# Optimization experiments

Hardware: AMD Instinct MI355X
Metric: run time of the kernel (lower is better)

Reference implementation:

```python
import jax, jax.numpy as jnp
import numpy as np

N = 12000
E = 384000
F_IN, F_HID, F_OUT = 4, 50, 1433
NEG_SLOPE = 0.2  # PyG GATConv default leaky_relu slope


def gat_conv(x, W, a_src, a_dst, b, src, dst):
    """PyG GATConv (heads=1, concat=True) with self-loops already appended.
    x: [N, Fin], W: [Fin, Fout], a_src/a_dst/b: [Fout], src/dst: [E']."""
    h = x @ W                                   # [N, Fout]
    al = h @ a_src                              # [N] per-source logit part
    ar = h @ a_dst                              # [N] per-target logit part
    e = jax.nn.leaky_relu(al[src] + ar[dst], NEG_SLOPE)   # [E'] edge logits
    # segment softmax over edges grouped by destination node
    m = jax.ops.segment_max(e, dst, num_segments=N)       # [N]
    ex = jnp.exp(e - m[dst])
    s = jax.ops.segment_sum(ex, dst, num_segments=N)      # [N]
    alpha = ex / s[dst]                         # [E'] (self-loops => s > 0)
    out = jax.ops.segment_sum(alpha[:, None] * h[src], dst, num_segments=N)
    return out + b


def setup_inputs() -> dict:
    key = jax.random.key(0)
    ks = jax.random.split(key, 10)
    x = jax.random.normal(ks[0], (N, F_IN), dtype=jnp.float32)
    edge_index = jax.random.randint(ks[1], (2, E), 0, N, dtype=jnp.int32)
    # Glorot-ish init for params
    W1 = jax.random.normal(ks[2], (F_IN, F_HID), dtype=jnp.float32) / np.sqrt(F_IN)
    a_src1 = jax.random.normal(ks[3], (F_HID,), dtype=jnp.float32) / np.sqrt(F_HID)
    a_dst1 = jax.random.normal(ks[4], (F_HID,), dtype=jnp.float32) / np.sqrt(F_HID)
    b1 = jnp.zeros((F_HID,), dtype=jnp.float32)
    W2 = jax.random.normal(ks[5], (F_HID, F_OUT), dtype=jnp.float32) / np.sqrt(F_HID)
    a_src2 = jax.random.normal(ks[6], (F_OUT,), dtype=jnp.float32) / np.sqrt(F_OUT)
    a_dst2 = jax.random.normal(ks[7], (F_OUT,), dtype=jnp.float32) / np.sqrt(F_OUT)
    b2 = jnp.zeros((F_OUT,), dtype=jnp.float32)
    return {"x": x, "edge_index": edge_index, "W1": W1, "a_src1": a_src1,
            "a_dst1": a_dst1, "b1": b1, "W2": W2, "a_src2": a_src2,
            "a_dst2": a_dst2, "b2": b2}


def reference(x, edge_index, W1, a_src1, a_dst1, b1, W2, a_src2, a_dst2, b2):
    # PyG GATConv adds self-loops by default
    loops = jnp.arange(N, dtype=edge_index.dtype)
    src = jnp.concatenate([edge_index[0], loops])
    dst = jnp.concatenate([edge_index[1], loops])
    h = jax.nn.relu(gat_conv(x, W1, a_src1, a_dst1, b1, src, dst))
    h = jax.nn.relu(gat_conv(h, W2, a_src2, a_dst2, b2, src, dst))
    adj_pred = jax.nn.sigmoid(h @ h.T)          # InnerProductDecoder.forward_all
    return (adj_pred, edge_index)
```

## Files before the change

kernel.cpp:

```cpp
#include <hip/hip_runtime.h>
#include <hip/hip_bf16.h>

#define NNODES 12000
#define NEDGES 384000
#define NETOT  (NEDGES + NNODES)
#define FIN    4
#define FHID   50
#define FOUT   1433
#define KP     1440
#define MP     12032
#define GT     (MP / 256)
#define GTRI   (GT * (GT + 1) / 2)
#define NEG_SLOPE 0.2f

typedef __hip_bfloat16 bf16_t;
typedef __bf16 bf16x8 __attribute__((ext_vector_type(8)));
typedef float f32x4 __attribute__((ext_vector_type(4)));
typedef float f32x2 __attribute__((ext_vector_type(2)));

__device__ __forceinline__ float  b2f(bf16_t h) { return __bfloat162float(h); }
__device__ __forceinline__ bf16_t f2b(float f)  { return __float2bfloat16(f); }
__device__ __forceinline__ unsigned short f2bu(float f) { bf16_t h = f2b(f); return *(unsigned short*)&h; }

__global__ void k_init(int* __restrict__ deg, bf16_t* __restrict__ h2) {
    int i = blockIdx.x * blockDim.x + threadIdx.x;
    int stride = gridDim.x * blockDim.x;
    for (int v = i; v < NNODES; v += stride) deg[v] = 1;
    const size_t padN = (size_t)(MP - NNODES) * KP;
    for (size_t t = i; t < padN; t += stride) h2[(size_t)NNODES * KP + t] = f2b(0.f);
}

__global__ void k_count(const int* __restrict__ ei, int* __restrict__ deg) {
    int i = blockIdx.x * blockDim.x + threadIdx.x;
    if (i < NEDGES) atomicAdd(&deg[ei[NEDGES + i]], 1);
}

__global__ __launch_bounds__(1024) void k_scan(const int* __restrict__ deg,
                                               int* __restrict__ rowptr,
                                               int* __restrict__ cursor) {
    __shared__ int wsum[16];
    const int tid = threadIdx.x, lane = tid & 63, wv = tid >> 6;
    const int base = tid * 12;
    int pref[12];
    int s = 0;
#pragma unroll
    for (int u = 0; u < 12; ++u) {
        int idx = base + u;
        int d = (idx < NNODES) ? deg[idx] : 0;
        pref[u] = s;
        s += d;
    }
    int sc = s;
#pragma unroll
    for (int o = 1; o < 64; o <<= 1) {
        int t2 = __shfl_up(sc, o, 64);
        if (lane >= o) sc += t2;
    }
    if (lane == 63) wsum[wv] = sc;
    __syncthreads();
    if (wv == 0 && lane < 16) {
        int mine = wsum[lane];
        int scw = mine;
#pragma unroll
        for (int o = 1; o < 16; o <<= 1) {
            int t3 = __shfl_up(scw, o, 64);
            if (lane >= o) scw += t3;
        }
        wsum[lane] = scw - mine;
    }
    __syncthreads();
    const int pre = wsum[wv] + (sc - s);
#pragma unroll
    for (int u = 0; u < 12; ++u) {
        int idx = base + u;
        if (idx < NNODES) {
            int p = pre + pref[u];
            rowptr[idx] = p;
            cursor[idx] = p;
        }
    }
    if (tid == 1023) rowptr[NNODES] = pre + s;
}

__global__ void k_fill(const int* __restrict__ ei, int* __restrict__ cursor,
                       int* __restrict__ csrc, float* __restrict__ outbase) {
    int i = blockIdx.x * blockDim.x + threadIdx.x;
    if (i < NETOT) {
        int s, d;
        if (i < NEDGES) { s = ei[i]; d = ei[NEDGES + i]; }
        else            { s = d = i - NEDGES; }
        int pos = atomicAdd(&cursor[d], 1);
        csrc[pos] = s;
    }
    if (i < 2 * NEDGES)
        outbase[(size_t)NNODES * (size_t)NNODES + (size_t)i] = (float)ei[i];
}

__global__ __launch_bounds__(256) void k_linear1(
        const bf16_t* __restrict__ x, const bf16_t* __restrict__ W1,
        const bf16_t* __restrict__ as1, const bf16_t* __restrict__ ad1,
        float* __restrict__ h1pre, float* __restrict__ al, float* __restrict__ ar) {
    __shared__ float sW[FIN * FHID];
    __shared__ float sa[FHID], sdl[FHID];
    int tid = threadIdx.x;
    if (tid < FIN * FHID) sW[tid] = b2f(W1[tid]);
    if (tid < FHID) { sa[tid] = b2f(as1[tid]); sdl[tid] = b2f(ad1[tid]); }
    __syncthreads();
    int i = blockIdx.x * 256 + tid;
    if (i >= NNODES) return;
    float x0 = b2f(x[i * 4 + 0]), x1 = b2f(x[i * 4 + 1]);
    float x2 = b2f(x[i * 4 + 2]), x3 = b2f(x[i * 4 + 3]);
    float hal = 0.f, har = 0.f;
    for (int j = 0; j < FHID; ++j) {
        float h = x0 * sW[j] + x1 * sW[FHID + j] + x2 * sW[2 * FHID + j] + x3 * sW[3 * FHID + j];
        h1pre[(size_t)i * FHID + j] = h;
        hal += h * sa[j];
        har += h * sdl[j];
    }
    al[i] = hal; ar[i] = har;
}

__global__ __launch_bounds__(256) void k_agg1(
        const float* __restrict__ h1pre, const float* __restrict__ al, const float* __restrict__ ar,
        const int* __restrict__ rowptr, const int* __restrict__ csrc,
        const bf16_t* __restrict__ b1, float* __restrict__ h1) {
    const int wv = threadIdx.x >> 6, lane = threadIdx.x & 63;
    const int v = blockIdx.x * 4 + wv;
    const int s0 = rowptr[v], s1 = rowptr[v + 1];
    const float arv = ar[v];
    float acc = 0.f, ssum = 0.f;
    for (int base = s0; base < s1; base += 64) {
        int e = base + lane;
        float w = 0.f; int si = 0;
        if (e < s1) {
            si = csrc[e];
            float l = al[si] + arv;
            l = l > 0.f ? l : NEG_SLOPE * l;
            w = __expf(l);
        }
        ssum += w;
        int cnt = min(64, s1 - base);
#pragma unroll 4
        for (int j = 0; j < cnt; ++j) {
            float wj = __shfl(w, j, 64);
            int   sj = __shfl(si, j, 64);
            if (lane < FHID) acc += wj * h1pre[(size_t)sj * FHID + lane];
        }
    }
#pragma unroll
    for (int o = 32; o; o >>= 1) ssum += __shfl_xor(ssum, o, 64);
    if (lane < FHID) {
        float o2 = acc / ssum + b2f(b1[lane]);
        h1[(size_t)v * FHID + lane] = fmaxf(o2, 0.f);
    }
}

__global__ __launch_bounds__(256) void k_linear2(
        const float* __restrict__ h1, const bf16_t* __restrict__ W2,
        const bf16_t* __restrict__ as2, const bf16_t* __restrict__ ad2,
        unsigned char* __restrict__ h2pre, float* __restrict__ al2, float* __restrict__ ar2) {
    int v0 = blockIdx.x * 4, tid = threadIdx.x;
    __shared__ float sh[4][FHID];
    if (tid < 4 * FHID) sh[tid / FHID][tid % FHID] = h1[(size_t)v0 * FHID + tid];
    __syncthreads();
    float pal[4] = {0.f, 0.f, 0.f, 0.f}, par[4] = {0.f, 0.f, 0.f, 0.f};
#pragma unroll
    for (int i = 0; i < 3; ++i) {
        int f0 = i * 512 + 2 * tid;
        if (f0 < KP) {
            float d0[4] = {0.f, 0.f, 0.f, 0.f}, d1[4] = {0.f, 0.f, 0.f, 0.f};
            bool ok0 = f0 < FOUT, ok1 = f0 + 1 < FOUT;
            if (ok0) {
                int f1 = ok1 ? f0 + 1 : f0;
#pragma unroll 10
                for (int k = 0; k < FHID; ++k) {
                    float w0 = b2f(W2[k * FOUT + f0]);
                    float w1 = b2f(W2[k * FOUT + f1]);
#pragma unroll
                    for (int c = 0; c < 4; ++c) {
                        d0[c] += sh[c][k] * w0;
                        d1[c] += sh[c][k] * w1;
                    }
                }
                if (!ok1) { d1[0] = d1[1] = d1[2] = d1[3] = 0.f; }
                float sa0 = b2f(as2[f0]), sd0 = b2f(ad2[f0]);
                float sa1 = ok1 ? b2f(as2[f0 + 1]) : 0.f;
                float sd1 = ok1 ? b2f(ad2[f0 + 1]) : 0.f;
#pragma unroll
                for (int c = 0; c < 4; ++c) {
                    pal[c] += d0[c] * sa0 + d1[c] * sa1;
                    par[c] += d0[c] * sd0 + d1[c] * sd1;
                }
            }
#pragma unroll
            for (int c = 0; c < 4; ++c) {
                int pk = __builtin_amdgcn_cvt_pk_fp8_f32(d0[c], d1[c], 0, false);
                *(unsigned short*)(h2pre + (size_t)(v0 + c) * KP + f0) = (unsigned short)pk;
            }
        }
    }
#pragma unroll
    for (int off = 32; off; off >>= 1)
#pragma unroll
        for (int c = 0; c < 4; ++c) {
            pal[c] += __shfl_xor(pal[c], off, 64);
            par[c] += __shfl_xor(par[c], off, 64);
        }
    __shared__ float rA[4][4], rB[4][4];
    int wave = tid >> 6, lane = tid & 63;
    if (lane == 0)
#pragma unroll
        for (int c = 0; c < 4; ++c) { rA[wave][c] = pal[c]; rB[wave][c] = par[c]; }
    __syncthreads();
    if (tid < 4) {
        al2[v0 + tid] = rA[0][tid] + rA[1][tid] + rA[2][tid] + rA[3][tid];
        ar2[v0 + tid] = rB[0][tid] + rB[1][tid] + rB[2][tid] + rB[3][tid];
    }
}

__global__ __launch_bounds__(256) void k_agg2(
        const unsigned char* __restrict__ h2pre, const float* __restrict__ al, const float* __restrict__ ar,
        const int* __restrict__ rowptr, const int* __restrict__ csrc,
        const bf16_t* __restrict__ bias2, bf16_t* __restrict__ h2) {
    int v = blockIdx.x, tid = threadIdx.x;
    int s0 = rowptr[v], s1 = rowptr[v + 1];
    float arv = ar[v];
    int wave = tid >> 6, lane = tid & 63;

    float acc[8] = {0.f, 0.f, 0.f, 0.f, 0.f, 0.f, 0.f, 0.f};
    float ssum = 0.f;
    __shared__ float sw[256];
    __shared__ int ssrc[256];
    __shared__ float red[4];
    const bool act = tid < (KP / 8);
    for (int base = s0; base < s1; base += 256) {
        int e = base + tid;
        float w = 0.f; int si = 0;
        if (e < s1) {
            si = csrc[e];
            float l = al[si] + arv;
            l = l > 0.f ? l : NEG_SLOPE * l;
            w = __expf(l);
        }
        ssum += w;
        sw[tid] = w; ssrc[tid] = si;
        __syncthreads();
        int cnt = min(256, s1 - base);
        if (act) {
#pragma unroll 8
            for (int j = 0; j < cnt; ++j) {
                float wj = sw[j];
                const uint2* hp = (const uint2*)(h2pre + (size_t)ssrc[j] * KP);
                uint2 p = hp[tid];
                f32x2 e0 = __builtin_amdgcn_cvt_pk_f32_fp8(p.x, false);
                f32x2 e1 = __builtin_amdgcn_cvt_pk_f32_fp8(p.x, true);
                f32x2 e2 = __builtin_amdgcn_cvt_pk_f32_fp8(p.y, false);
                f32x2 e3 = __builtin_amdgcn_cvt_pk_f32_fp8(p.y, true);
                acc[0] += wj * e0.x; acc[1] += wj * e0.y;
                acc[2] += wj * e1.x; acc[3] += wj * e1.y;
                acc[4] += wj * e2.x; acc[5] += wj * e2.y;
                acc[6] += wj * e3.x; acc[7] += wj * e3.y;
            }
        }
        __syncthreads();
    }
#pragma unroll
    for (int off = 32; off; off >>= 1) ssum += __shfl_xor(ssum, off, 64);
    if (lane == 0) red[wave] = ssum;
    __syncthreads();
    float inv = 1.f / (red[0] + red[1] + red[2] + red[3]);

    if (act) {
        int fb = 8 * tid;
        unsigned short o[8];
#pragma unroll
        for (int t = 0; t < 8; ++t) {
            int f = fb + t;
            o[t] = f2bu((f < FOUT) ? fmaxf(acc[t] * inv + b2f(bias2[f]), 0.f) : 0.f);
        }
        uint4 pk;
        pk.x = (unsigned)o[0] | ((unsigned)o[1] << 16);
        pk.y = (unsigned)o[2] | ((unsigned)o[3] << 16);
        pk.z = (unsigned)o[4] | ((unsigned)o[5] << 16);
        pk.w = (unsigned)o[6] | ((unsigned)o[7] << 16);
        *(uint4*)(h2 + (size_t)v * KP + fb) = pk;
    }
}

__global__ __launch_bounds__(512, 2) void k_gemm_sig(const bf16_t* __restrict__ Hm,
                                                     float* __restrict__ out) {
    int t = blockIdx.x;
    int by = (int)((2 * GT + 1 - sqrtf((float)(2 * GT + 1) * (2 * GT + 1) - 8.0f * t)) * 0.5f);
    if (by < 0) by = 0;
    if (by > GT - 1) by = GT - 1;
    while (by + 1 < GT && (by + 1) * GT - ((by + 1) * by) / 2 <= t) ++by;
    while (by > 0 && by * GT - (by * (by - 1)) / 2 > t) --by;
    int bx = by + (t - (by * GT - (by * (by - 1)) / 2));

    __shared__ __align__(16) char ldsA[2 * 256 * 64 * 2];
    __shared__ __align__(16) char ldsB[2 * 256 * 64 * 2];

    const int tid  = threadIdx.x;
    const int wave = tid >> 6, lane = tid & 63;
    const int rowA0 = by * 256, rowB0 = bx * 256;

    const int phys  = wave * 1024 + lane * 16;
    const int physL = phys ^ (((phys >> 7) & 7) << 4);
    const int srow  = physL >> 7;
    const int scol  = (physL & 127) >> 1;
    const bf16_t* gA0 = Hm + (size_t)(rowA0 + srow) * KP + scol;
    const bf16_t* gB0 = Hm + (size_t)(rowB0 + srow) * KP + scol;

#define STAGE_TILE(slot_, kt_) do {                                            \
        char* la_ = ldsA + (slot_) * 32768 + wave * 1024;                      \
        char* lb_ = ldsB + (slot_) * 32768 + wave * 1024;                      \
        _Pragma("unroll")                                                      \
        for (int c_ = 0; c_ < 4; ++c_)                                         \
            __builtin_amdgcn_global_load_lds(                                  \
                (const __attribute__((address_space(1))) void*)(gA0 + (size_t)(c_ * 64) * KP + (kt_) * 64), \
                (__attribute__((address_space(3))) void*)(la_ + c_ * 8192), 16, 0, 0); \
        _Pragma("unroll")                                                      \
        for (int c_ = 0; c_ < 4; ++c_)                                         \
            __builtin_amdgcn_global_load_lds(                                  \
                (const __attribute__((address_space(1))) void*)(gB0 + (size_t)(c_ * 64) * KP + (kt_) * 64), \
                (__attribute__((address_space(3))) void*)(lb_ + c_ * 8192), 16, 0, 0); \
    } while (0)

    const int wr = wave >> 2, wc = wave & 3;
    const int r = lane & 15, q = lane >> 4;
    const int swz = (r & 7) << 4;
    const int aBase = wr * 16384 + r * 128;
    const int bBase = wc * 8192  + r * 128;

    f32x4 acc[8][4] = {};

    STAGE_TILE(0, 0);
    for (int kt = 0; kt < 22; ++kt) {
        if (kt < 21) {
            STAGE_TILE((kt + 1) & 1, kt + 1);
            __builtin_amdgcn_sched_barrier(0);
            asm volatile("s_waitcnt vmcnt(8)" ::: "memory");
        } else {
            __builtin_amdgcn_sched_barrier(0);
            asm volatile("s_waitcnt vmcnt(0)" ::: "memory");
        }
        __builtin_amdgcn_s_barrier();
        __builtin_amdgcn_sched_barrier(0);
        const char* Ab = ldsA + (kt & 1) * 32768;
        const char* Bb = ldsB + (kt & 1) * 32768;
#pragma unroll
        for (int ks = 0; ks < 2; ++ks) {
            const int cb = (ks * 64 + q * 16) ^ swz;
            bf16x8 af[8], bfr[4];
#pragma unroll
            for (int mi = 0; mi < 8; ++mi)
                af[mi] = *(const bf16x8*)(Ab + aBase + mi * 2048 + cb);
#pragma unroll
            for (int ni = 0; ni < 4; ++ni)
                bfr[ni] = *(const bf16x8*)(Bb + bBase + ni * 2048 + cb);
#pragma unroll
            for (int mi = 0; mi < 8; ++mi)
#pragma unroll
                for (int ni = 0; ni < 4; ++ni)
                    acc[mi][ni] = __builtin_amdgcn_mfma_f32_16x16x32_bf16(af[mi], bfr[ni], acc[mi][ni], 0, 0, 0);
        }
        __builtin_amdgcn_sched_barrier(0);
        __builtin_amdgcn_s_barrier();
        __builtin_amdgcn_sched_barrier(0);
    }
#undef STAGE_TILE

    {
        bf16x8 at[8], bt[4];
#pragma unroll
        for (int mi = 0; mi < 8; ++mi)
            at[mi] = *(const bf16x8*)(Hm + (size_t)(rowA0 + wr * 128 + mi * 16 + r) * KP + 1408 + q * 8);
#pragma unroll
        for (int ni = 0; ni < 4; ++ni)
            bt[ni] = *(const bf16x8*)(Hm + (size_t)(rowB0 + wc * 64 + ni * 16 + r) * KP + 1408 + q * 8);
#pragma unroll
        for (int mi = 0; mi < 8; ++mi)
#pragma unroll
            for (int ni = 0; ni < 4; ++ni)
                acc[mi][ni] = __builtin_amdgcn_mfma_f32_16x16x32_bf16(at[mi], bt[ni], acc[mi][ni], 0, 0, 0);
    }

#pragma unroll
    for (int mi = 0; mi < 8; ++mi) {
        const int row0 = rowA0 + wr * 128 + mi * 16 + q * 4;
#pragma unroll
        for (int ni = 0; ni < 4; ++ni) {
            const int col = rowB0 + wc * 64 + ni * 16 + r;
            if (col < NNODES && row0 < NNODES) {
                f32x4 s;
#pragma unroll
                for (int r2 = 0; r2 < 4; ++r2)
                    s[r2] = 1.f / (1.f + __expf(-acc[mi][ni][r2]));
#pragma unroll
                for (int r2 = 0; r2 < 4; ++r2)
                    out[(size_t)(row0 + r2) * NNODES + col] = s[r2];
                if (bx != by)
                    *(f32x4*)(out + (size_t)col * NNODES + row0) = s;
            }
        }
    }
}

extern "C" void kernel_launch(void* const* d_in, const int* in_sizes, int n_in,
                              void* d_out, int out_size, void* d_ws, size_t ws_size,
                              hipStream_t stream) {
    const bf16_t* x   = (const bf16_t*)d_in[0];
    const int*    ei  = (const int*)d_in[1];
    const bf16_t* W1  = (const bf16_t*)d_in[2];
    const bf16_t* as1 = (const bf16_t*)d_in[3];
    const bf16_t* ad1 = (const bf16_t*)d_in[4];
    const bf16_t* b1  = (const bf16_t*)d_in[5];
    const bf16_t* W2  = (const bf16_t*)d_in[6];
    const bf16_t* as2 = (const bf16_t*)d_in[7];
    const bf16_t* ad2 = (const bf16_t*)d_in[8];
    const bf16_t* b2  = (const bf16_t*)d_in[9];
    float* out = (float*)d_out;

    char* obuf = (char*)d_out;
    size_t off = 0;
    auto carve = [&](size_t bytes) {
        char* p = obuf + off;
        off += (bytes + 255) & ~(size_t)255;
        return p;
    };
    float* h1pre  = (float*)carve((size_t)NNODES * FHID * 4);
    float* al1    = (float*)carve((size_t)NNODES * 4);
    float* ar1    = (float*)carve((size_t)NNODES * 4);
    float* h1     = (float*)carve((size_t)NNODES * FHID * 4);
    float* al2    = (float*)carve((size_t)NNODES * 4);
    float* ar2    = (float*)carve((size_t)NNODES * 4);
    int*   deg    = (int*)carve((size_t)NNODES * 4);
    int*   rowptr = (int*)carve((size_t)(NNODES + 1) * 4);
    int*   cursor = (int*)carve((size_t)NNODES * 4);
    int*   csrc   = (int*)carve((size_t)NETOT * 4);
    unsigned char* h2pre = (unsigned char*)carve((size_t)NNODES * KP);
    bf16_t* h2 = (bf16_t*)d_ws;
    (void)ws_size; (void)in_sizes; (void)n_in; (void)out_size;

    hipLaunchKernelGGL(k_init,    dim3(256), dim3(256), 0, stream, deg, h2);
    hipLaunchKernelGGL(k_count,   dim3((NEDGES + 255) / 256), dim3(256), 0, stream, ei, deg);
    hipLaunchKernelGGL(k_scan,    dim3(1), dim3(1024), 0, stream, deg, rowptr, cursor);
    hipLaunchKernelGGL(k_fill,    dim3((2 * NEDGES + 255) / 256), dim3(256), 0, stream,
                       ei, cursor, csrc, out);
    hipLaunchKernelGGL(k_linear1, dim3((NNODES + 255) / 256), dim3(256), 0, stream,
                       x, W1, as1, ad1, h1pre, al1, ar1);
    hipLaunchKernelGGL(k_agg1,    dim3(NNODES / 4), dim3(256), 0, stream,
                       h1pre, al1, ar1, rowptr, csrc, b1, h1);
    hipLaunchKernelGGL(k_linear2, dim3(NNODES / 4), dim3(256), 0, stream,
                       h1, W2, as2, ad2, h2pre, al2, ar2);
    hipLaunchKernelGGL(k_agg2,    dim3(NNODES), dim3(256), 0, stream,
                       h2pre, al2, ar2, rowptr, csrc, b2, h2);
    hipLaunchKernelGGL(k_gemm_sig, dim3(GTRI), dim3(512), 0, stream, h2, out);
}
```

Baseline: 1.149 ms.

## Restructure bf16 GEMM main loop into split-K staged ping-pong with XCD-aware tile remap

Measured after the change: 1.134 ms. About the same (-1.3%).

```diff
diff --git a/kernel.cpp b/kernel.cpp
--- a/kernel.cpp
+++ b/kernel.cpp
@@ -289,95 +289,99 @@
 
 __global__ __launch_bounds__(512, 2) void k_gemm_sig(const bf16_t* __restrict__ Hm,
                                                      float* __restrict__ out) {
-    int t = blockIdx.x;
-    int by = (int)((2 * GT + 1 - sqrtf((float)(2 * GT + 1) * (2 * GT + 1) - 8.0f * t)) * 0.5f);
+    int t0 = (blockIdx.x & 7) * (GTRI / 8) + (blockIdx.x >> 3);
+    int by = (int)((2 * GT + 1 - sqrtf((float)(2 * GT + 1) * (2 * GT + 1) - 8.0f * t0)) * 0.5f);
     if (by < 0) by = 0;
     if (by > GT - 1) by = GT - 1;
-    while (by + 1 < GT && (by + 1) * GT - ((by + 1) * by) / 2 <= t) ++by;
-    while (by > 0 && by * GT - (by * (by - 1)) / 2 > t) --by;
-    int bx = by + (t - (by * GT - (by * (by - 1)) / 2));
-
-    __shared__ __align__(16) char ldsA[2 * 256 * 64 * 2];
-    __shared__ __align__(16) char ldsB[2 * 256 * 64 * 2];
+    while (by + 1 < GT && (by + 1) * GT - ((by + 1) * by) / 2 <= t0) ++by;
+    while (by > 0 && by * GT - (by * (by - 1)) / 2 > t0) --by;
+    int bx = by + (t0 - (by * GT - (by * (by - 1)) / 2));
+
+    __shared__ __align__(16) char lds[131072];
 
     const int tid  = threadIdx.x;
     const int wave = tid >> 6, lane = tid & 63;
     const int rowA0 = by * 256, rowB0 = bx * 256;
-
-    const int phys  = wave * 1024 + lane * 16;
-    const int physL = phys ^ (((phys >> 7) & 7) << 4);
-    const int srow  = physL >> 7;
-    const int scol  = (physL & 127) >> 1;
-    const bf16_t* gA0 = Hm + (size_t)(rowA0 + srow) * KP + scol;
-    const bf16_t* gB0 = Hm + (size_t)(rowB0 + srow) * KP + scol;
-
-#define STAGE_TILE(slot_, kt_) do {                                            \
-        char* la_ = ldsA + (slot_) * 32768 + wave * 1024;                      \
-        char* lb_ = ldsB + (slot_) * 32768 + wave * 1024;                      \
-        _Pragma("unroll")                                                      \
-        for (int c_ = 0; c_ < 4; ++c_)                                         \
-            __builtin_amdgcn_global_load_lds(                                  \
-                (const __attribute__((address_space(1))) void*)(gA0 + (size_t)(c_ * 64) * KP + (kt_) * 64), \
-                (__attribute__((address_space(3))) void*)(la_ + c_ * 8192), 16, 0, 0); \
-        _Pragma("unroll")                                                      \
-        for (int c_ = 0; c_ < 4; ++c_)                                         \
-            __builtin_amdgcn_global_load_lds(                                  \
-                (const __attribute__((address_space(1))) void*)(gB0 + (size_t)(c_ * 64) * KP + (kt_) * 64), \
-                (__attribute__((address_space(3))) void*)(lb_ + c_ * 8192), 16, 0, 0); \
+    const int wr = wave >> 2, wc = wave & 3;
+    const int r = lane & 15, q4 = lane >> 4;
+
+    const int lin  = wave * 1024 + lane * 16;
+    const int grow = lin >> 6;
+    const int gcol = (lin & 63) >> 1;
+    const bf16_t* gAs = Hm + (size_t)(rowA0 + grow) * KP + gcol;
+    const bf16_t* gBs = Hm + (size_t)(rowB0 + grow) * KP + gcol;
+
+    const int aOff = (wr * 128 + r) * 64 + q4 * 16;
+    const int bOff = (wc * 64  + r) * 64 + q4 * 16;
+
+    f32x4 acc[8][4] = {};
+    bf16x8 af[4], bfr[4];
+
+#define STAGE_KH(ns_, kt_, kh_) do {                                             \
+        const bf16_t* gs_ = ((kh_) & 1) ? gBs : gAs;                             \
+        char* ld_ = lds + (ns_) * 65536 + ((kh_) & 1) * 32768                    \
+                        + ((kh_) >> 1) * 16384 + wave * 1024;                    \
+        const int kc_ = (kt_) * 64 + ((kh_) >> 1) * 32;                          \
+        __builtin_amdgcn_global_load_lds(                                        \
+            (const __attribute__((address_space(1))) void*)(gs_ + kc_),          \
+            (__attribute__((address_space(3))) void*)ld_, 16, 0, 0);             \
+        __builtin_amdgcn_global_load_lds(                                        \
+            (const __attribute__((address_space(1))) void*)(gs_ + kc_ + (size_t)128 * KP), \
+            (__attribute__((address_space(3))) void*)(ld_ + 8192), 16, 0, 0);    \
     } while (0)
 
-    const int wr = wave >> 2, wc = wave & 3;
-    const int r = lane & 15, q = lane >> 4;
-    const int swz = (r & 7) << 4;
-    const int aBase = wr * 16384 + r * 128;
-    const int bBase = wc * 8192  + r * 128;
-
-    f32x4 acc[8][4] = {};
-
-    STAGE_TILE(0, 0);
-    for (int kt = 0; kt < 22; ++kt) {
-        if (kt < 21) {
-            STAGE_TILE((kt + 1) & 1, kt + 1);
-            __builtin_amdgcn_sched_barrier(0);
-            asm volatile("s_waitcnt vmcnt(8)" ::: "memory");
-        } else {
-            __builtin_amdgcn_sched_barrier(0);
-            asm volatile("s_waitcnt vmcnt(0)" ::: "memory");
-        }
-        __builtin_amdgcn_s_barrier();
-        __builtin_amdgcn_sched_barrier(0);
-        const char* Ab = ldsA + (kt & 1) * 32768;
-        const char* Bb = ldsB + (kt & 1) * 32768;
-#pragma unroll
-        for (int ks = 0; ks < 2; ++ks) {
-            const int cb = (ks * 64 + q * 16) ^ swz;
-            bf16x8 af[8], bfr[4];
-#pragma unroll
-            for (int mi = 0; mi < 8; ++mi)
-                af[mi] = *(const bf16x8*)(Ab + aBase + mi * 2048 + cb);
-#pragma unroll
-            for (int ni = 0; ni < 4; ++ni)
-                bfr[ni] = *(const bf16x8*)(Bb + bBase + ni * 2048 + cb);
-#pragma unroll
-            for (int mi = 0; mi < 8; ++mi)
-#pragma unroll
-                for (int ni = 0; ni < 4; ++ni)
-                    acc[mi][ni] = __builtin_amdgcn_mfma_f32_16x16x32_bf16(af[mi], bfr[ni], acc[mi][ni], 0, 0, 0);
-        }
-        __builtin_amdgcn_sched_barrier(0);
-        __builtin_amdgcn_s_barrier();
-        __builtin_amdgcn_sched_barrier(0);
-    }
-#undef STAGE_TILE
+#define LOAD_BFR(Bb_, ks_) { _Pragma("unroll") for (int n_ = 0; n_ < 4; ++n_)    \
+        bfr[n_] = *(const bf16x8*)((Bb_) + (ks_) * 16384 + bOff + n_ * 1024); }
+#define LOAD_AF(Ab_, ks_, mh_) { _Pragma("unroll") for (int m_ = 0; m_ < 4; ++m_) \
+        af[m_] = *(const bf16x8*)((Ab_) + (ks_) * 16384 + aOff + (mh_) * 4096 + m_ * 1024); }
+
+#define MFMA16(mh_) {                                                            \
+        __builtin_amdgcn_s_setprio(1);                                           \
+        _Pragma("unroll") for (int m_ = 0; m_ < 4; ++m_)                         \
+        _Pragma("unroll") for (int n_ = 0; n_ < 4; ++n_)                         \
+            acc[(mh_) * 4 + m_][n_] = __builtin_amdgcn_mfma_f32_16x16x32_bf16(   \
+                af[m_], bfr[n_], acc[(mh_) * 4 + m_][n_], 0, 0, 0);              \
+        __builtin_amdgcn_s_setprio(0); }
+
+#define SYNC_PRE()  { __builtin_amdgcn_s_barrier();                              \
+        asm volatile("s_waitcnt lgkmcnt(0)" ::: "memory");                       \
+        __builtin_amdgcn_sched_barrier(0); }
+#define SYNC_POST() { __builtin_amdgcn_sched_barrier(0); __builtin_amdgcn_s_barrier(); }
+
+    STAGE_KH(0, 0, 0); STAGE_KH(0, 0, 1); STAGE_KH(0, 0, 2); STAGE_KH(0, 0, 3);
+    asm volatile("s_waitcnt vmcnt(4)" ::: "memory");
+    __builtin_amdgcn_s_barrier();
+
+#pragma unroll 1
+    for (int t = 0; t < 22; ++t) {
+        const int sl = t & 1, ns = sl ^ 1;
+        const char* Ab = lds + sl * 65536;
+        const char* Bb = lds + sl * 65536 + 32768;
+        const bool st = (t < 21);
+        LOAD_BFR(Bb, 0); LOAD_AF(Ab, 0, 0);
+        if (st) STAGE_KH(ns, t + 1, 0);
+        SYNC_PRE(); MFMA16(0); SYNC_POST();
+        LOAD_AF(Ab, 0, 1);
+        if (st) { STAGE_KH(ns, t + 1, 1); asm volatile("s_waitcnt vmcnt(4)" ::: "memory"); }
+        else    { asm volatile("s_waitcnt vmcnt(0)" ::: "memory"); }
+        SYNC_PRE(); MFMA16(1); SYNC_POST();
+        LOAD_BFR(Bb, 1); LOAD_AF(Ab, 1, 0);
+        if (st) STAGE_KH(ns, t + 1, 2);
+        SYNC_PRE(); MFMA16(0); SYNC_POST();
+        LOAD_AF(Ab, 1, 1);
+        if (st) { STAGE_KH(ns, t + 1, 3); asm volatile("s_waitcnt vmcnt(4)" ::: "memory"); }
+        SYNC_PRE(); MFMA16(1); SYNC_POST();
+    }
+#undef STAGE_KH
 
     {
         bf16x8 at[8], bt[4];
 #pragma unroll
         for (int mi = 0; mi < 8; ++mi)
-            at[mi] = *(const bf16x8*)(Hm + (size_t)(rowA0 + wr * 128 + mi * 16 + r) * KP + 1408 + q * 8);
+            at[mi] = *(const bf16x8*)(Hm + (size_t)(rowA0 + wr * 128 + mi * 16 + r) * KP + 1408 + q4 * 8);
 #pragma unroll
         for (int ni = 0; ni < 4; ++ni)
-            bt[ni] = *(const bf16x8*)(Hm + (size_t)(rowB0 + wc * 64 + ni * 16 + r) * KP + 1408 + q * 8);
+            bt[ni] = *(const bf16x8*)(Hm + (size_t)(rowB0 + wc * 64 + ni * 16 + r) * KP + 1408 + q4 * 8);
 #pragma unroll
         for (int mi = 0; mi < 8; ++mi)
 #pragma unroll
@@ -387,7 +391,7 @@
 
 #pragma unroll
     for (int mi = 0; mi < 8; ++mi) {
-        const int row0 = rowA0 + wr * 128 + mi * 16 + q * 4;
+        const int row0 = rowA0 + wr * 128 + mi * 16 + q4 * 4;
 #pragma unroll
         for (int ni = 0; ni < 4; ++ni) {
             const int col = rowB0 + wc * 64 + ni * 16 + r;
```
